# Kernel tuning notes

Measured on AMD Instinct MI355X. Metric: run time of the kernel, lower is better.

## Reference

```python
import jax, jax.numpy as jnp
import numpy as np

E, N = 400000, 50000
D = 128          # efeat_dim = src_dim = dst_dim = output_dim
H = 512          # hidden_dim
CAT = 3 * D      # concat of [efeat, src, dst]
LN_EPS = 1e-5


def setup_inputs() -> dict:
    key = jax.random.key(0)
    ks = jax.random.split(key, 12)
    scale = 0.02
    return {
        "efeat": jax.random.normal(ks[0], (E, D), jnp.float32),
        "src_feat": jax.random.normal(ks[1], (N, D), jnp.float32),
        "dst_feat": jax.random.normal(ks[2], (N, D), jnp.float32),
        "src_idx": jax.random.randint(ks[3], (E,), 0, N),
        "dst_idx": jax.random.randint(ks[4], (E,), 0, N),
        # MLP params: Linear(CAT,H) -> SiLU -> Linear(H,H) -> SiLU -> Linear(H,D) -> LayerNorm(D)
        "W1": jax.random.normal(ks[5], (CAT, H), jnp.float32) * scale,
        "b1": jnp.zeros((H,), jnp.float32),
        "W2": jax.random.normal(ks[6], (H, H), jnp.float32) * scale,
        "b2": jnp.zeros((H,), jnp.float32),
        "W3": jax.random.normal(ks[7], (H, D), jnp.float32) * scale,
        "b3": jnp.zeros((D,), jnp.float32),
        "gamma": jnp.ones((D,), jnp.float32),
        "beta": jnp.zeros((D,), jnp.float32),
    }


def _layer_norm(y, gamma, beta):
    mu = jnp.mean(y, axis=-1, keepdims=True)
    var = jnp.mean(jnp.square(y - mu), axis=-1, keepdims=True)
    return (y - mu) * jax.lax.rsqrt(var + LN_EPS) * gamma + beta


def reference(efeat, src_feat, dst_feat, src_idx, dst_idx,
              W1, b1, W2, b2, W3, b3, gamma, beta):
    # concat_efeat: per-edge gather of src/dst node feats + concat with edge feats
    cat = jnp.concatenate([efeat, src_feat[src_idx], dst_feat[dst_idx]], axis=1)  # [E, 3D]
    h = jax.nn.silu(cat @ W1 + b1)   # [E, H]
    h = jax.nn.silu(h @ W2 + b2)     # [E, H]
    y = h @ W3 + b3                  # [E, D]
    return _layer_norm(y, gamma, beta)
```

## Files before the change

kernel.cpp:

```cpp
#include <hip/hip_runtime.h>
#include <hip/hip_bf16.h>
#include <cstdint>
#include <cstddef>

typedef __attribute__((ext_vector_type(4))) float f32x4;
typedef __attribute__((ext_vector_type(8))) short s16x8;
typedef __attribute__((ext_vector_type(4))) unsigned int u32x4;

#define E_ 400000
#define D_ 128
#define H_ 512
#define CAT_ 384
#define BM 64
#define NBLK 6250
#define SCRATCH 65536
#define LDS_TOTAL (65536 + 1024)

__device__ __forceinline__ unsigned cvtpk(float lo, float hi) {
  unsigned r;
  asm("v_cvt_pk_bf16_f32 %0, %1, %2" : "=v"(r) : "v"(lo), "v"(hi));
  return r;
}
__device__ __forceinline__ float silu_f(float x) {
  return x * __builtin_amdgcn_rcpf(1.0f + __expf(-x));
}

#define HS(row, byteoff) (smem + (row) * 1024 + ((byteoff) ^ (((row) & 7) << 4)))

__global__ __launch_bounds__(512, 4)
void edge_mlp_fused(const float* __restrict__ efeat,
                    const float* __restrict__ src_feat,
                    const float* __restrict__ dst_feat,
                    const int* __restrict__ src_idx,
                    const int* __restrict__ dst_idx,
                    const unsigned short* __restrict__ P1,
                    const unsigned short* __restrict__ P2,
                    const unsigned short* __restrict__ P3,
                    const float* __restrict__ b1,
                    const float* __restrict__ b2,
                    const float* __restrict__ b3,
                    const float* __restrict__ gamma,
                    const float* __restrict__ beta,
                    float* __restrict__ out) {
  extern __shared__ char smem[];
  const int tid = threadIdx.x;
  const int lane = tid & 63;
  const int wave = tid >> 6;
  const int lr = lane & 15;
  const int kc = lane >> 4;
  const int g4 = kc * 4;
  const size_t e0 = (size_t)blockIdx.x * BM;

  const unsigned short* w1base = P1 + (size_t)kc * 4096 + wave * 512 + lr * 8;
  const unsigned short* w2base = P2 + (size_t)kc * 4096 + wave * 512 + lr * 8;

  const int grow = tid >> 3, gq = tid & 7;
  const size_t ee = e0 + grow;

#define LOAD4(dst, base) { const float* s0_ = (base) + gq * 8; \
  dst[0] = *(const f32x4*)s0_;        dst[1] = *(const f32x4*)(s0_ + 4); \
  dst[2] = *(const f32x4*)(s0_ + 64); dst[3] = *(const f32x4*)(s0_ + 68); }

#define STASH(v, scol) { \
  u32x4 r0_, r1_; \
  r0_.x = cvtpk(v[0][0], v[0][1]); r0_.y = cvtpk(v[0][2], v[0][3]); \
  r0_.z = cvtpk(v[1][0], v[1][1]); r0_.w = cvtpk(v[1][2], v[1][3]); \
  r1_.x = cvtpk(v[2][0], v[2][1]); r1_.y = cvtpk(v[2][2], v[2][3]); \
  r1_.z = cvtpk(v[3][0], v[3][1]); r1_.w = cvtpk(v[3][2], v[3][3]); \
  *(u32x4*)HS(grow, ((scol) + gq * 8) * 2) = r0_; \
  *(u32x4*)HS(grow, ((scol) + 64 + gq * 8) * 2) = r1_; }

  {
    f32x4 acc[4][4];
    #pragma unroll
    for (int eg = 0; eg < 4; ++eg)
      #pragma unroll
      for (int j = 0; j < 4; ++j) acc[eg][j] = (f32x4){0.f, 0.f, 0.f, 0.f};

    const float* psrc = src_feat + (size_t)src_idx[ee] * D_;
    const float* pdst = dst_feat + (size_t)dst_idx[ee] * D_;

    f32x4 gs[4], gx[4];
    LOAD4(gs, psrc);
    LOAD4(gx, efeat + ee * D_);
    STASH(gx, 0);

    asm volatile("s_waitcnt lgkmcnt(0)" ::: "memory");
    __builtin_amdgcn_s_barrier();
    asm volatile("" ::: "memory");

    auto g1tier = [&](int P0) {
      #pragma unroll
      for (int pp = 0; pp < 4; ++pp) {
        const int p = P0 + pp;
        s16x8 w[4];
        #pragma unroll
        for (int j = 0; j < 4; ++j)
          w[j] = *(const s16x8*)(w1base + (size_t)p * 16384 + j * 128);
        #pragma unroll
        for (int eg = 0; eg < 4; ++eg) {
          const s16x8 bf = *(const s16x8*)HS(eg * 16 + lr, p * 64 + kc * 16);
          #pragma unroll
          for (int j = 0; j < 4; ++j)
            acc[eg][j] = __builtin_amdgcn_mfma_f32_16x16x32_bf16(w[j], bf, acc[eg][j], 0, 0, 0);
        }
      }
    };

    g1tier(0);
    STASH(gs, 128);
    LOAD4(gx, pdst);
    asm volatile("s_waitcnt lgkmcnt(0)" ::: "memory");
    __builtin_amdgcn_s_barrier();
    asm volatile("" ::: "memory");

    g1tier(4);
    STASH(gx, 256);
    asm volatile("s_waitcnt lgkmcnt(0)" ::: "memory");
    __builtin_amdgcn_s_barrier();
    asm volatile("" ::: "memory");

    g1tier(8);

    __builtin_amdgcn_s_barrier();
    asm volatile("" ::: "memory");

    #pragma unroll
    for (int j = 0; j < 4; ++j) {
      const int col0 = (wave * 4 + j) * 16 + g4;
      const f32x4 bv = *(const f32x4*)(b1 + col0);
      #pragma unroll
      for (int eg = 0; eg < 4; ++eg) {
        uint2 o_;
        o_.x = cvtpk(silu_f(acc[eg][j][0] + bv[0]), silu_f(acc[eg][j][1] + bv[1]));
        o_.y = cvtpk(silu_f(acc[eg][j][2] + bv[2]), silu_f(acc[eg][j][3] + bv[3]));
        *(uint2*)HS(eg * 16 + lr, col0 * 2) = o_;
      }
    }
  }
  asm volatile("s_waitcnt lgkmcnt(0)" ::: "memory");
  __builtin_amdgcn_s_barrier();
  asm volatile("" ::: "memory");

  {
    f32x4 acc[4][4];
    #pragma unroll
    for (int eg = 0; eg < 4; ++eg)
      #pragma unroll
      for (int j = 0; j < 4; ++j) acc[eg][j] = (f32x4){0.f, 0.f, 0.f, 0.f};

    #pragma unroll 2
    for (int p = 0; p < 16; ++p) {
      s16x8 w[4];
      #pragma unroll
      for (int j = 0; j < 4; ++j)
        w[j] = *(const s16x8*)(w2base + (size_t)p * 16384 + j * 128);
      #pragma unroll
      for (int eg = 0; eg < 4; ++eg) {
        const s16x8 bf = *(const s16x8*)HS(eg * 16 + lr, p * 64 + kc * 16);
        #pragma unroll
        for (int j = 0; j < 4; ++j)
          acc[eg][j] = __builtin_amdgcn_mfma_f32_16x16x32_bf16(w[j], bf, acc[eg][j], 0, 0, 0);
      }
    }

    __builtin_amdgcn_s_barrier();
    asm volatile("" ::: "memory");

    #pragma unroll
    for (int j = 0; j < 4; ++j) {
      const int col0 = (wave * 4 + j) * 16 + g4;
      const f32x4 bv = *(const f32x4*)(b2 + col0);
      #pragma unroll
      for (int eg = 0; eg < 4; ++eg) {
        uint2 o_;
        o_.x = cvtpk(silu_f(acc[eg][j][0] + bv[0]), silu_f(acc[eg][j][1] + bv[1]));
        o_.y = cvtpk(silu_f(acc[eg][j][2] + bv[2]), silu_f(acc[eg][j][3] + bv[3]));
        *(uint2*)HS(eg * 16 + lr, col0 * 2) = o_;
      }
    }
  }
  asm volatile("s_waitcnt lgkmcnt(0)" ::: "memory");
  __builtin_amdgcn_s_barrier();
  asm volatile("" ::: "memory");

  {
    const int eg3 = wave >> 1;
    const int half = wave & 1;
    const int edge = eg3 * 16 + lr;

    f32x4 acc[4];
    #pragma unroll
    for (int j = 0; j < 4; ++j) acc[j] = (f32x4){0.f, 0.f, 0.f, 0.f};

    const unsigned short* w3b = P3 + (size_t)kc * 1024 + half * 512 + lr * 8;

    #pragma unroll 2
    for (int p = 0; p < 16; ++p) {
      s16x8 w[4];
      #pragma unroll
      for (int j = 0; j < 4; ++j)
        w[j] = *(const s16x8*)(w3b + (size_t)p * 4096 + j * 128);
      const s16x8 bf = *(const s16x8*)HS(edge, p * 64 + kc * 16);
      #pragma unroll
      for (int j = 0; j < 4; ++j)
        acc[j] = __builtin_amdgcn_mfma_f32_16x16x32_bf16(w[j], bf, acc[j], 0, 0, 0);
    }

    float sum = 0.f, ss = 0.f;
    #pragma unroll
    for (int j = 0; j < 4; ++j) {
      const f32x4 bv = *(const f32x4*)(b3 + half * 64 + j * 16 + g4);
      #pragma unroll
      for (int r = 0; r < 4; ++r) {
        acc[j][r] += bv[r];
        sum += acc[j][r];
        ss += acc[j][r] * acc[j][r];
      }
    }
    sum += __shfl_xor(sum, 16, 64); ss += __shfl_xor(ss, 16, 64);
    sum += __shfl_xor(sum, 32, 64); ss += __shfl_xor(ss, 32, 64);

    if (lane < 16) {
      float2 pw; pw.x = sum; pw.y = ss;
      *(float2*)(smem + SCRATCH + edge * 16 + half * 8) = pw;
    }
    asm volatile("s_waitcnt lgkmcnt(0)" ::: "memory");
    __builtin_amdgcn_s_barrier();
    asm volatile("" ::: "memory");

    const f32x4 pt = *(const f32x4*)(smem + SCRATCH + edge * 16);
    const float sumT = pt[0] + pt[2];
    const float ssT  = pt[1] + pt[3];
    const float mu = sumT * (1.0f / 128.0f);
    const float var = ssT * (1.0f / 128.0f) - mu * mu;
    const float rstd = rsqrtf(var + 1e-5f);

    float* orow = out + (e0 + edge) * D_ + half * 64;
    #pragma unroll
    for (int j = 0; j < 4; ++j) {
      const f32x4 gv  = *(const f32x4*)(gamma + half * 64 + j * 16 + g4);
      const f32x4 btv = *(const f32x4*)(beta  + half * 64 + j * 16 + g4);
      f32x4 o;
      #pragma unroll
      for (int r = 0; r < 4; ++r)
        o[r] = (acc[j][r] - mu) * rstd * gv[r] + btv[r];
      *(f32x4*)(orow + j * 16 + g4) = o;
    }
  }
#undef LOAD4
#undef STASH
}

__global__ void prep_pack(const float* __restrict__ W, unsigned short* __restrict__ P,
                          int K, int N) {
  const int t = blockIdx.x * blockDim.x + threadIdx.x;
  if (t >= N * (K >> 3)) return;
  const int n = t % N;
  const int k8 = t / N;
  const int k0 = k8 << 3;
  const int p = k0 >> 5, kc = (k0 >> 3) & 3;
  s16x8 w;
  #pragma unroll
  for (int j = 0; j < 8; ++j) {
    union { float f; unsigned u; } t_; t_.f = W[(size_t)(k0 + j) * N + n];
    w[j] = (short)((t_.u + 0x8000u) >> 16);
  }
  *(s16x8*)(P + (size_t)p * N * 32 + (size_t)kc * N * 8 + (size_t)n * 8) = w;
}

extern "C" void kernel_launch(void* const* d_in, const int* in_sizes, int n_in,
                              void* d_out, int out_size, void* d_ws, size_t ws_size,
                              hipStream_t stream) {
  const float* efeat    = (const float*)d_in[0];
  const float* src_feat = (const float*)d_in[1];
  const float* dst_feat = (const float*)d_in[2];
  const int*   src_idx  = (const int*)d_in[3];
  const int*   dst_idx  = (const int*)d_in[4];
  const float* W1 = (const float*)d_in[5];
  const float* b1 = (const float*)d_in[6];
  const float* W2 = (const float*)d_in[7];
  const float* b2 = (const float*)d_in[8];
  const float* W3 = (const float*)d_in[9];
  const float* b3 = (const float*)d_in[10];
  const float* gamma = (const float*)d_in[11];
  const float* beta  = (const float*)d_in[12];

  unsigned short* P1 = (unsigned short*)d_ws;
  unsigned short* P2 = P1 + 196608;
  unsigned short* P3 = P2 + 262144;

  (void)hipFuncSetAttribute((const void*)edge_mlp_fused,
                            hipFuncAttributeMaxDynamicSharedMemorySize, LDS_TOTAL);

  prep_pack<<<(512 * 48 + 255) / 256, 256, 0, stream>>>(W1, P1, CAT_, H_);
  prep_pack<<<(512 * 64 + 255) / 256, 256, 0, stream>>>(W2, P2, H_, H_);
  prep_pack<<<(128 * 64 + 255) / 256, 256, 0, stream>>>(W3, P3, H_, D_);

  edge_mlp_fused<<<NBLK, 512, LDS_TOTAL, stream>>>(
      efeat, src_feat, dst_feat, src_idx, dst_idx,
      P1, P2, P3, b1, b2, b3, gamma, beta, (float*)d_out);
}
```

Before: 562.2 us.

## Switch MLP GEMMs to 32x32x16 bf16 MFMA with repacked weights

```diff
diff --git a/kernel.cpp b/kernel.cpp
--- a/kernel.cpp
+++ b/kernel.cpp
@@ -4,6 +4,7 @@
 #include <cstddef>
 
 typedef __attribute__((ext_vector_type(4))) float f32x4;
+typedef __attribute__((ext_vector_type(16))) float f32x16;
 typedef __attribute__((ext_vector_type(8))) short s16x8;
 typedef __attribute__((ext_vector_type(4))) unsigned int u32x4;
 
@@ -14,7 +15,7 @@
 #define BM 64
 #define NBLK 6250
 #define SCRATCH 65536
-#define LDS_TOTAL (65536 + 1024)
+#define LDS_TOTAL (65536 + 2048)
 
 __device__ __forceinline__ unsigned cvtpk(float lo, float hi) {
   unsigned r;
@@ -46,13 +47,10 @@
   const int tid = threadIdx.x;
   const int lane = tid & 63;
   const int wave = tid >> 6;
-  const int lr = lane & 15;
-  const int kc = lane >> 4;
-  const int g4 = kc * 4;
+  const int l31 = lane & 31;
+  const int kh = lane >> 5;
   const size_t e0 = (size_t)blockIdx.x * BM;
-
-  const unsigned short* w1base = P1 + (size_t)kc * 4096 + wave * 512 + lr * 8;
-  const unsigned short* w2base = P2 + (size_t)kc * 4096 + wave * 512 + lr * 8;
+  const int rot = ((blockIdx.x >> 8) & 1) << 4;
 
   const int grow = tid >> 3, gq = tid & 7;
   const size_t ee = e0 + grow;
@@ -70,40 +68,65 @@
   *(u32x4*)HS(grow, ((scol) + gq * 8) * 2) = r0_; \
   *(u32x4*)HS(grow, ((scol) + 64 + gq * 8) * 2) = r1_; }
 
+  const unsigned short* w1base = P1 + (size_t)kh * (H_ * 8) + (wave * 64 + l31) * 8;
+  const unsigned short* w2base = P2 + (size_t)kh * (H_ * 8) + (wave * 64 + l31) * 8;
+
+#define SILU_STORE(acc, bias) { \
+    _Pragma("unroll") \
+    for (int t = 0; t < 2; ++t) { \
+      _Pragma("unroll") \
+      for (int g = 0; g < 4; ++g) { \
+        const int col0 = wave * 64 + t * 32 + g * 8 + kh * 4; \
+        const f32x4 bv = *(const f32x4*)((bias) + col0); \
+        _Pragma("unroll") \
+        for (int et = 0; et < 2; ++et) { \
+          uint2 o_; \
+          o_.x = cvtpk(silu_f(acc[t][et][g * 4 + 0] + bv[0]), silu_f(acc[t][et][g * 4 + 1] + bv[1])); \
+          o_.y = cvtpk(silu_f(acc[t][et][g * 4 + 2] + bv[2]), silu_f(acc[t][et][g * 4 + 3] + bv[3])); \
+          *(uint2*)HS(et * 32 + l31, col0 * 2) = o_; \
+        } \
+      } \
+    } }
+
   {
-    f32x4 acc[4][4];
-    #pragma unroll
-    for (int eg = 0; eg < 4; ++eg)
-      #pragma unroll
-      for (int j = 0; j < 4; ++j) acc[eg][j] = (f32x4){0.f, 0.f, 0.f, 0.f};
+    f32x16 acc[2][2];
+    #pragma unroll
+    for (int t = 0; t < 2; ++t)
+      #pragma unroll
+      for (int et = 0; et < 2; ++et)
+        #pragma unroll
+        for (int r = 0; r < 16; ++r) acc[t][et][r] = 0.f;
 
     const float* psrc = src_feat + (size_t)src_idx[ee] * D_;
     const float* pdst = dst_feat + (size_t)dst_idx[ee] * D_;
 
-    f32x4 gs[4], gx[4];
+    f32x4 gx[4], gs[4];
+    LOAD4(gx, efeat + ee * D_);
     LOAD4(gs, psrc);
-    LOAD4(gx, efeat + ee * D_);
     STASH(gx, 0);
 
     asm volatile("s_waitcnt lgkmcnt(0)" ::: "memory");
     __builtin_amdgcn_s_barrier();
     asm volatile("" ::: "memory");
 
-    auto g1tier = [&](int P0) {
-      #pragma unroll
-      for (int pp = 0; pp < 4; ++pp) {
-        const int p = P0 + pp;
-        s16x8 w[4];
-        #pragma unroll
-        for (int j = 0; j < 4; ++j)
-          w[j] = *(const s16x8*)(w1base + (size_t)p * 16384 + j * 128);
-        #pragma unroll
-        for (int eg = 0; eg < 4; ++eg) {
-          const s16x8 bf = *(const s16x8*)HS(eg * 16 + lr, p * 64 + kc * 16);
+    auto g1tier = [&](int S0) {
+      const unsigned short* wp = w1base + (size_t)S0 * (H_ * 16);
+      #pragma unroll 1
+      for (int pp = 0; pp < 8; ++pp) {
+        const int s = S0 + pp;
+        s16x8 w[2], bf[2];
+        #pragma unroll
+        for (int t = 0; t < 2; ++t)
+          w[t] = *(const s16x8*)(wp + t * 256);
+        #pragma unroll
+        for (int et = 0; et < 2; ++et)
+          bf[et] = *(const s16x8*)HS(et * 32 + l31, s * 32 + kh * 16);
+        #pragma unroll
+        for (int t = 0; t < 2; ++t)
           #pragma unroll
-          for (int j = 0; j < 4; ++j)
-            acc[eg][j] = __builtin_amdgcn_mfma_f32_16x16x32_bf16(w[j], bf, acc[eg][j], 0, 0, 0);
-        }
+          for (int et = 0; et < 2; ++et)
+            acc[t][et] = __builtin_amdgcn_mfma_f32_32x32x16_bf16(w[t], bf[et], acc[t][et], 0, 0, 0);
+        wp += H_ * 16;
       }
     };
 
@@ -114,142 +137,127 @@
     __builtin_amdgcn_s_barrier();
     asm volatile("" ::: "memory");
 
-    g1tier(4);
+    g1tier(8);
     STASH(gx, 256);
     asm volatile("s_waitcnt lgkmcnt(0)" ::: "memory");
     __builtin_amdgcn_s_barrier();
     asm volatile("" ::: "memory");
 
-    g1tier(8);
-
-    __builtin_amdgcn_s_barrier();
-    asm volatile("" ::: "memory");
-
-    #pragma unroll
-    for (int j = 0; j < 4; ++j) {
-      const int col0 = (wave * 4 + j) * 16 + g4;
-      const f32x4 bv = *(const f32x4*)(b1 + col0);
-      #pragma unroll
-      for (int eg = 0; eg < 4; ++eg) {
-        uint2 o_;
-        o_.x = cvtpk(silu_f(acc[eg][j][0] + bv[0]), silu_f(acc[eg][j][1] + bv[1]));
-        o_.y = cvtpk(silu_f(acc[eg][j][2] + bv[2]), silu_f(acc[eg][j][3] + bv[3]));
-        *(uint2*)HS(eg * 16 + lr, col0 * 2) = o_;
-      }
-    }
+    g1tier(16);
+
+    __builtin_amdgcn_s_barrier();
+    asm volatile("" ::: "memory");
+
+    SILU_STORE(acc, b1);
   }
   asm volatile("s_waitcnt lgkmcnt(0)" ::: "memory");
   __builtin_amdgcn_s_barrier();
   asm volatile("" ::: "memory");
 
   {
-    f32x4 acc[4][4];
-    #pragma unroll
-    for (int eg = 0; eg < 4; ++eg)
-      #pragma unroll
-      for (int j = 0; j < 4; ++j) acc[eg][j] = (f32x4){0.f, 0.f, 0.f, 0.f};
+    f32x16 acc[2][2];
+    #pragma unroll
+    for (int t = 0; t < 2; ++t)
+      #pragma unroll
+      for (int et = 0; et < 2; ++et)
+        #pragma unroll
+        for (int r = 0; r < 16; ++r) acc[t][et][r] = 0.f;
 
     #pragma unroll 2
-    for (int p = 0; p < 16; ++p) {
-      s16x8 w[4];
-      #pragma unroll
-      for (int j = 0; j < 4; ++j)
-        w[j] = *(const s16x8*)(w2base + (size_t)p * 16384 + j * 128);
-      #pragma unroll
-      for (int eg = 0; eg < 4; ++eg) {
-        const s16x8 bf = *(const s16x8*)HS(eg * 16 + lr, p * 64 + kc * 16);
-        #pragma unroll
-        for (int j = 0; j < 4; ++j)
-          acc[eg][j] = __builtin_amdgcn_mfma_f32_16x16x32_bf16(w[j], bf, acc[eg][j], 0, 0, 0);
-      }
-    }
-
-    __builtin_amdgcn_s_barrier();
-    asm volatile("" ::: "memory");
-
-    #pragma unroll
-    for (int j = 0; j < 4; ++j) {
-      const int col0 = (wave * 4 + j) * 16 + g4;
-      const f32x4 bv = *(const f32x4*)(b2 + col0);
-      #pragma unroll
-      for (int eg = 0; eg < 4; ++eg) {
-        uint2 o_;
-        o_.x = cvtpk(silu_f(acc[eg][j][0] + bv[0]), silu_f(acc[eg][j][1] + bv[1]));
-        o_.y = cvtpk(silu_f(acc[eg][j][2] + bv[2]), silu_f(acc[eg][j][3] + bv[3]));
-        *(uint2*)HS(eg * 16 + lr, col0 * 2) = o_;
-      }
-    }
+    for (int pp = 0; pp < 32; ++pp) {
+      const int s = (pp + rot) & 31;
+      s16x8 w[2], bf[2];
+      #pragma unroll
+      for (int t = 0; t < 2; ++t)
+        w[t] = *(const s16x8*)(w2base + (size_t)s * (H_ * 16) + t * 256);
+      #pragma unroll
+      for (int et = 0; et < 2; ++et)
+        bf[et] = *(const s16x8*)HS(et * 32 + l31, s * 32 + kh * 16);
+      #pragma unroll
+      for (int t = 0; t < 2; ++t)
+        #pragma unroll
+        for (int et = 0; et < 2; ++et)
+          acc[t][et] = __builtin_amdgcn_mfma_f32_32x32x16_bf16(w[t], bf[et], acc[t][et], 0, 0, 0);
+    }
+
+    __builtin_amdgcn_s_barrier();
+    asm volatile("" ::: "memory");
+
+    SILU_STORE(acc, b2);
   }
   asm volatile("s_waitcnt lgkmcnt(0)" ::: "memory");
   __builtin_amdgcn_s_barrier();
   asm volatile("" ::: "memory");
 
   {
-    const int eg3 = wave >> 1;
-    const int half = wave & 1;
-    const int edge = eg3 * 16 + lr;
-
-    f32x4 acc[4];
-    #pragma unroll
-    for (int j = 0; j < 4; ++j) acc[j] = (f32x4){0.f, 0.f, 0.f, 0.f};
-
-    const unsigned short* w3b = P3 + (size_t)kc * 1024 + half * 512 + lr * 8;
+    const int colt = wave & 3;
+    const int et3 = wave >> 2;
+    const int edge = et3 * 32 + l31;
+
+    f32x16 accA, accB;
+    #pragma unroll
+    for (int r = 0; r < 16; ++r) { accA[r] = 0.f; accB[r] = 0.f; }
+
+    const unsigned short* w3b = P3 + (size_t)kh * (D_ * 8) + (colt * 32 + l31) * 8;
 
     #pragma unroll 2
-    for (int p = 0; p < 16; ++p) {
-      s16x8 w[4];
-      #pragma unroll
-      for (int j = 0; j < 4; ++j)
-        w[j] = *(const s16x8*)(w3b + (size_t)p * 4096 + j * 128);
-      const s16x8 bf = *(const s16x8*)HS(edge, p * 64 + kc * 16);
-      #pragma unroll
-      for (int j = 0; j < 4; ++j)
-        acc[j] = __builtin_amdgcn_mfma_f32_16x16x32_bf16(w[j], bf, acc[j], 0, 0, 0);
-    }
+    for (int pp = 0; pp < 32; pp += 2) {
+      const int s0 = (pp + rot) & 31;
+      const int s1 = (pp + 1 + rot) & 31;
+      const s16x8 wA = *(const s16x8*)(w3b + (size_t)s0 * (D_ * 16));
+      const s16x8 bA = *(const s16x8*)HS(edge, s0 * 32 + kh * 16);
+      accA = __builtin_amdgcn_mfma_f32_32x32x16_bf16(wA, bA, accA, 0, 0, 0);
+      const s16x8 wB = *(const s16x8*)(w3b + (size_t)s1 * (D_ * 16));
+      const s16x8 bB = *(const s16x8*)HS(edge, s1 * 32 + kh * 16);
+      accB = __builtin_amdgcn_mfma_f32_32x32x16_bf16(wB, bB, accB, 0, 0, 0);
+    }
+    #pragma unroll
+    for (int r = 0; r < 16; ++r) accA[r] += accB[r];
 
     float sum = 0.f, ss = 0.f;
     #pragma unroll
-    for (int j = 0; j < 4; ++j) {
-      const f32x4 bv = *(const f32x4*)(b3 + half * 64 + j * 16 + g4);
+    for (int g = 0; g < 4; ++g) {
+      const f32x4 bv = *(const f32x4*)(b3 + colt * 32 + g * 8 + kh * 4);
       #pragma unroll
       for (int r = 0; r < 4; ++r) {
-        acc[j][r] += bv[r];
-        sum += acc[j][r];
-        ss += acc[j][r] * acc[j][r];
+        accA[g * 4 + r] += bv[r];
+        sum += accA[g * 4 + r];
+        ss += accA[g * 4 + r] * accA[g * 4 + r];
       }
     }
-    sum += __shfl_xor(sum, 16, 64); ss += __shfl_xor(ss, 16, 64);
     sum += __shfl_xor(sum, 32, 64); ss += __shfl_xor(ss, 32, 64);
 
-    if (lane < 16) {
+    if (lane < 32) {
       float2 pw; pw.x = sum; pw.y = ss;
-      *(float2*)(smem + SCRATCH + edge * 16 + half * 8) = pw;
+      *(float2*)(smem + SCRATCH + edge * 32 + colt * 8) = pw;
     }
     asm volatile("s_waitcnt lgkmcnt(0)" ::: "memory");
     __builtin_amdgcn_s_barrier();
     asm volatile("" ::: "memory");
 
-    const f32x4 pt = *(const f32x4*)(smem + SCRATCH + edge * 16);
-    const float sumT = pt[0] + pt[2];
-    const float ssT  = pt[1] + pt[3];
+    const f32x4 pa = *(const f32x4*)(smem + SCRATCH + edge * 32);
+    const f32x4 pb = *(const f32x4*)(smem + SCRATCH + edge * 32 + 16);
+    const float sumT = pa[0] + pa[2] + pb[0] + pb[2];
+    const float ssT  = pa[1] + pa[3] + pb[1] + pb[3];
     const float mu = sumT * (1.0f / 128.0f);
     const float var = ssT * (1.0f / 128.0f) - mu * mu;
     const float rstd = rsqrtf(var + 1e-5f);
 
-    float* orow = out + (e0 + edge) * D_ + half * 64;
-    #pragma unroll
-    for (int j = 0; j < 4; ++j) {
-      const f32x4 gv  = *(const f32x4*)(gamma + half * 64 + j * 16 + g4);
-      const f32x4 btv = *(const f32x4*)(beta  + half * 64 + j * 16 + g4);
+    float* orow = out + (e0 + edge) * D_ + colt * 32 + kh * 4;
+    #pragma unroll
+    for (int g = 0; g < 4; ++g) {
+      const f32x4 gv  = *(const f32x4*)(gamma + colt * 32 + g * 8 + kh * 4);
+      const f32x4 btv = *(const f32x4*)(beta  + colt * 32 + g * 8 + kh * 4);
       f32x4 o;
       #pragma unroll
       for (int r = 0; r < 4; ++r)
-        o[r] = (acc[j][r] - mu) * rstd * gv[r] + btv[r];
-      *(f32x4*)(orow + j * 16 + g4) = o;
+        o[r] = (accA[g * 4 + r] - mu) * rstd * gv[r] + btv[r];
+      *(f32x4*)(orow + g * 8) = o;
     }
   }
 #undef LOAD4
 #undef STASH
+#undef SILU_STORE
 }
 
 __global__ void prep_pack(const float* __restrict__ W, unsigned short* __restrict__ P,
@@ -259,14 +267,14 @@
   const int n = t % N;
   const int k8 = t / N;
   const int k0 = k8 << 3;
-  const int p = k0 >> 5, kc = (k0 >> 3) & 3;
+  const int s = k0 >> 4, khp = (k0 >> 3) & 1;
   s16x8 w;
   #pragma unroll
   for (int j = 0; j < 8; ++j) {
     union { float f; unsigned u; } t_; t_.f = W[(size_t)(k0 + j) * N + n];
     w[j] = (short)((t_.u + 0x8000u) >> 16);
   }
-  *(s16x8*)(P + (size_t)p * N * 32 + (size_t)kc * N * 8 + (size_t)n * 8) = w;
+  *(s16x8*)(P + (size_t)s * N * 16 + (size_t)khp * N * 8 + (size_t)n * 8) = w;
 }
 
 extern "C" void kernel_launch(void* const* d_in, const int* in_sizes, int n_in,
```

Measured after the change: 571.1 us. No clear change (+1.6%).
